# Performance work log

Measured on AMD Instinct MI355X. Metric: run time of the kernel, lower is better.

The kernel has to match this reference:

```python
import jax, jax.numpy as jnp
import numpy as np

NUM_SHARED = 2
NUM_EXPERTS = 8
NUM_LOCAL = NUM_EXPERTS - NUM_SHARED
TOP_K = 2
BALANCE_COEFF = 0.1
INPUT_DIM = 256
HIDDEN_DIM = 512
PRED_LEN = 256
NUM_SCALES = 3


def _gelu(v):
    return jax.nn.gelu(v, approximate=False)  # torch nn.GELU default = exact erf


def setup_inputs() -> dict:
    key = jax.random.key(0)
    ks = iter(jax.random.split(key, 32))
    s = 0.02

    def w(shape):
        return jax.random.normal(next(ks), shape, dtype=jnp.float32) * s

    inp = {}
    inp["xs"] = jax.random.normal(next(ks), (NUM_SCALES, 32, 512, INPUT_DIM), dtype=jnp.float32)
    # router: Linear(E, 2E) -> GELU -> Linear(2E, num_experts) -> softmax
    inp["router_w1"] = w((INPUT_DIM, 2 * INPUT_DIM)); inp["router_b1"] = jnp.zeros((2 * INPUT_DIM,), jnp.float32)
    inp["router_w2"] = w((2 * INPUT_DIM, NUM_EXPERTS)); inp["router_b2"] = jnp.zeros((NUM_EXPERTS,), jnp.float32)
    # global experts (3-layer MLP), stacked over num_shared
    inp["gW1"] = w((NUM_SHARED, INPUT_DIM, HIDDEN_DIM)); inp["gb1"] = jnp.zeros((NUM_SHARED, HIDDEN_DIM), jnp.float32)
    inp["gW2"] = w((NUM_SHARED, HIDDEN_DIM, HIDDEN_DIM)); inp["gb2"] = jnp.zeros((NUM_SHARED, HIDDEN_DIM), jnp.float32)
    inp["gW3"] = w((NUM_SHARED, HIDDEN_DIM, PRED_LEN)); inp["gb3"] = jnp.zeros((NUM_SHARED, PRED_LEN), jnp.float32)
    # local experts (2-layer MLP), stacked over num_local
    inp["lW1"] = w((NUM_LOCAL, INPUT_DIM, HIDDEN_DIM)); inp["lb1"] = jnp.zeros((NUM_LOCAL, HIDDEN_DIM), jnp.float32)
    inp["lW2"] = w((NUM_LOCAL, HIDDEN_DIM, PRED_LEN)); inp["lb2"] = jnp.zeros((NUM_LOCAL, PRED_LEN), jnp.float32)
    # TemporalAwareWeighting
    inp["te_w"] = w((PRED_LEN, PRED_LEN)); inp["te_b"] = jnp.zeros((PRED_LEN,), jnp.float32)
    inp["weight_memory"] = jnp.zeros((1, NUM_SCALES), jnp.float32)
    inp["wc_w"] = w((PRED_LEN * NUM_SCALES + NUM_SCALES, NUM_SCALES)); inp["wc_b"] = jnp.zeros((NUM_SCALES,), jnp.float32)
    # output layer
    inp["out_w1"] = w((PRED_LEN, PRED_LEN)); inp["out_b1"] = jnp.zeros((PRED_LEN,), jnp.float32)
    inp["out_w2"] = w((PRED_LEN, PRED_LEN)); inp["out_b2"] = jnp.zeros((PRED_LEN,), jnp.float32)
    return inp


def reference(xs, router_w1, router_b1, router_w2, router_b2,
              gW1, gb1, gW2, gb2, gW3, gb3,
              lW1, lb1, lW2, lb2,
              te_w, te_b, weight_memory, wc_w, wc_b,
              out_w1, out_b1, out_w2, out_b2):
    S, B, C, E = xs.shape
    x = xs.reshape(S, B * C, E)

    def scale_fwd(xf):  # xf: [T, E]
        h = _gelu(xf @ router_w1 + router_b1)
        w = jax.nn.softmax(h @ router_w2 + router_b2, axis=-1)  # [T, Ne]
        gw = w[:, :NUM_SHARED]
        lw, lidx = jax.lax.top_k(w[:, NUM_SHARED:], TOP_K)      # sorted desc, like torch.topk
        # global experts: all run, weighted sum
        gh = _gelu(jnp.einsum('te,seh->sth', xf, gW1) + gb1[:, None, :])
        gh = _gelu(jnp.einsum('sth,shg->stg', gh, gW2) + gb2[:, None, :])
        gout = jnp.einsum('stg,sgo->sto', gh, gW3) + gb3[:, None, :]   # [Ns, T, O]
        global_pred = jnp.einsum('sto,ts->to', gout, gw)
        # local experts: all run (as in source), then top-k gather
        lh = _gelu(jnp.einsum('te,neh->nth', xf, lW1) + lb1[:, None, :])
        lout = jnp.einsum('nth,nho->nto', lh, lW2) + lb2[:, None, :]   # [Nl, T, O]
        sel = jnp.take_along_axis(jnp.swapaxes(lout, 0, 1), lidx[:, :, None], axis=1)  # [T, k, O]
        local_pred = jnp.sum(sel * lw[:, :, None], axis=1)
        return global_pred + local_pred, w

    preds, all_w = jax.vmap(scale_fwd)(x)  # [S, T, O], [S, T, Ne]

    ws = all_w.reshape(-1, all_w.shape[-1])
    entropy = -jnp.mean(jnp.sum(ws * jnp.log(ws + 1e-8), axis=-1))
    balance_loss = BALANCE_COEFF * entropy

    preds_bc = preds.reshape(S, B, C, -1)
    # TemporalAwareWeighting (dropout = identity in eval)
    reprs = _gelu(jnp.mean(preds_bc, axis=2) @ te_w + te_b)            # [S, B, O]
    concat = jnp.transpose(reprs, (1, 0, 2)).reshape(B, -1)            # [B, S*O]
    mem = jnp.broadcast_to(weight_memory, (B, S))
    raw = jax.nn.softplus(jnp.tanh(jnp.concatenate([concat, mem], axis=-1) @ wc_w + wc_b))
    sw = jax.nn.softmax(raw, axis=-1)                                  # [B, S]

    weighted = jnp.einsum('sbco,bs->bco', preds_bc, sw)
    out = _gelu(weighted @ out_w1 + out_b1) @ out_w2 + out_b2
    return out, balance_loss
```

## Files before the change

kernel.cpp:

```cpp
#include <hip/hip_runtime.h>
#include <hip/hip_bf16.h>
#include <math.h>

#define S_   3
#define B_   32
#define C_   512
#define E_   256
#define H_   512
#define P_   256
#define T_   49152
#define TBC_ 16384

typedef __attribute__((ext_vector_type(8))) short v_s16x8;
typedef __attribute__((ext_vector_type(4))) float v_f32x4;

__device__ __forceinline__ float gelu_f(float x) {
  return 0.5f * x * (1.0f + erff(x * 0.70710678118654752440f));
}

__device__ __forceinline__ void gload_lds16(const void* g, void* l) {
  __builtin_amdgcn_global_load_lds((const __attribute__((address_space(1))) void*)g,
                                   (__attribute__((address_space(3))) void*)l, 16, 0, 0);
}

template<int MODE, bool STORE, bool SPLITA>
__global__ __launch_bounds__(256)
void gemm_bf16_k(const __hip_bfloat16* __restrict__ A,
                 const __hip_bfloat16* __restrict__ Bt,
                 const float* __restrict__ bias,
                 void* __restrict__ Cout,
                 const float* __restrict__ wtok,
                 int M, int N, int K, int eidx,
                 const __hip_bfloat16* __restrict__ Alo)
{
  __shared__ __align__(16) unsigned short As[4096];
  __shared__ __align__(16) unsigned short Bs[4096];
  const int tid  = threadIdx.x;
  const int wid  = tid >> 6;
  const int lane = tid & 63;
  const int wm = wid >> 1, wn = wid & 1;
  const int l15 = lane & 15, l4 = lane >> 4;

  v_f32x4 acc[4][4] = {};

  const size_t Kb   = (size_t)K * 2;
  const size_t ArsB = SPLITA ? 512 : Kb;
  const char* AgHi = (const char*)A + (size_t)blockIdx.x * 128 * ArsB;
  const char* AgLo = SPLITA ? ((const char*)Alo + (size_t)blockIdx.x * 128 * ArsB) : nullptr;
  const char* Bg   = (const char*)Bt + (size_t)blockIdx.y * 128 * Kb;

  const int ob0 = (0 * 4 + wid) * 1024 + lane * 16;
  const int ob1 = (1 * 4 + wid) * 1024 + lane * 16;
  const int r0 = ob0 >> 6, kb0 = ob0 & 63;
  const int r1 = ob1 >> 6, kb1 = ob1 & 63;
  char* lA0 = (char*)As + (0 * 4 + wid) * 1024;
  char* lA1 = (char*)As + (1 * 4 + wid) * 1024;
  char* lB0 = (char*)Bs + (0 * 4 + wid) * 1024;
  char* lB1 = (char*)Bs + (1 * 4 + wid) * 1024;
  const size_t aoff0 = (size_t)r0 * ArsB + kb0;
  const size_t aoff1 = (size_t)r1 * ArsB + kb1;
  const char* gB0 = Bg + (size_t)r0 * Kb + kb0;
  const char* gB1 = Bg + (size_t)r1 * Kb + kb1;

  for (int kt = 0; kt < K; kt += 32) {
    const char* Asrc = AgHi;
    size_t akt = (size_t)kt * 2;
    if (SPLITA) {
      akt = (size_t)(kt & 255) * 2;
      if ((kt >> 8) == 1) Asrc = AgLo;
    }
    size_t bkt = (size_t)kt * 2;
    gload_lds16(Asrc + aoff0 + akt, lA0);
    gload_lds16(Asrc + aoff1 + akt, lA1);
    gload_lds16(gB0 + bkt, lB0);
    gload_lds16(gB1 + bkt, lB1);
    __syncthreads();
    v_s16x8 af[4], bfv[4];
#pragma unroll
    for (int m = 0; m < 4; ++m)
      af[m] = *(const v_s16x8*)(As + (wm * 64 + m * 16 + l15) * 32 + l4 * 8);
#pragma unroll
    for (int n = 0; n < 4; ++n)
      bfv[n] = *(const v_s16x8*)(Bs + (wn * 64 + n * 16 + l15) * 32 + l4 * 8);
#pragma unroll
    for (int m = 0; m < 4; ++m)
#pragma unroll
      for (int n = 0; n < 4; ++n)
        acc[m][n] = __builtin_amdgcn_mfma_f32_16x16x32_bf16(af[m], bfv[n], acc[m][n], 0, 0, 0);
    __syncthreads();
  }

  const int crow0 = blockIdx.x * 128 + wm * 64;
  const int ccol0 = blockIdx.y * 128 + wn * 64;
#pragma unroll
  for (int m = 0; m < 4; ++m) {
    float wv[4];
    if (MODE == 1) {
#pragma unroll
      for (int j = 0; j < 4; ++j)
        wv[j] = wtok[(size_t)(crow0 + m * 16 + l4 * 4 + j) * 8 + eidx];
    }
#pragma unroll
    for (int n = 0; n < 4; ++n) {
      const int col = ccol0 + n * 16 + l15;
      const float bv = bias[col];
#pragma unroll
      for (int j = 0; j < 4; ++j) {
        const int row = crow0 + m * 16 + l4 * 4 + j;
        float v = acc[m][n][j] + bv;
        if (MODE == 0) {
          ((__hip_bfloat16*)Cout)[(size_t)row * N + col] = __float2bfloat16(gelu_f(v));
        } else if (MODE == 1) {
          float* Pp = (float*)Cout + (size_t)row * N + col;
          float val = v * wv[j];
          if (STORE) *Pp = val; else *Pp += val;
        } else if (MODE == 2) {
          ((float*)Cout)[(size_t)row * N + col] = v;
        } else {
          ((float*)Cout)[(size_t)row * N + col] = gelu_f(v);
        }
      }
    }
  }
}

__global__ __launch_bounds__(256) void logits_kernel(
    const float* __restrict__ hr,
    const float* __restrict__ w2,
    const float* __restrict__ b2,
    float* __restrict__ wtok,
    float* __restrict__ entp)
{
  const int t = blockIdx.x * 256 + threadIdx.x;
  const float4* hrow = (const float4*)(hr + (size_t)t * 512);
  float lg[8];
#pragma unroll
  for (int e = 0; e < 8; ++e) lg[e] = b2[e];
#pragma unroll 4
  for (int k4 = 0; k4 < 128; ++k4) {
    float4 hv = hrow[k4];
    float hvv[4] = {hv.x, hv.y, hv.z, hv.w};
#pragma unroll
    for (int j = 0; j < 4; ++j) {
      const float* wr = w2 + (k4 * 4 + j) * 8;
#pragma unroll
      for (int e = 0; e < 8; ++e) lg[e] += hvv[j] * wr[e];
    }
  }
  float we[8];
  float mx = lg[0];
#pragma unroll
  for (int e = 1; e < 8; ++e) mx = fmaxf(mx, lg[e]);
  float ssum = 0.f;
#pragma unroll
  for (int e = 0; e < 8; ++e) { we[e] = expf(lg[e] - mx); ssum += we[e]; }
#pragma unroll
  for (int e = 0; e < 8; ++e) we[e] = we[e] / ssum;
  float ent = 0.f;
#pragma unroll
  for (int e = 0; e < 8; ++e) ent += we[e] * logf(we[e] + 1e-8f);
  int i1 = 0; float v1 = we[2];
#pragma unroll
  for (int n = 1; n < 6; ++n) if (we[2 + n] > v1) { v1 = we[2 + n]; i1 = n; }
  int i2 = -1; float v2 = -1e30f;
#pragma unroll
  for (int n = 0; n < 6; ++n) if (n != i1 && we[2 + n] > v2) { v2 = we[2 + n]; i2 = n; }
  float ow[8];
  ow[0] = we[0]; ow[1] = we[1];
#pragma unroll
  for (int n = 0; n < 6; ++n) ow[2 + n] = 0.f;
  ow[2 + i1] = v1; ow[2 + i2] = v2;
  float* wp = wtok + (size_t)t * 8;
#pragma unroll
  for (int e = 0; e < 8; ++e) wp[e] = ow[e];
  __shared__ float red[256];
  red[threadIdx.x] = ent;
  __syncthreads();
  for (int s = 128; s > 0; s >>= 1) {
    if (threadIdx.x < s) red[threadIdx.x] += red[threadIdx.x + s];
    __syncthreads();
  }
  if (threadIdx.x == 0) atomicAdd(entp, red[0]);
}

__global__ void zero_kernel(float* p) { p[0] = 0.f; }

__global__ void convert_x_kernel(const float* __restrict__ x,
                                 __hip_bfloat16* __restrict__ xb,
                                 __hip_bfloat16* __restrict__ xlo, int n4) {
  int stride = gridDim.x * blockDim.x;
  for (int i = blockIdx.x * blockDim.x + threadIdx.x; i < n4; i += stride) {
    float4 v = ((const float4*)x)[i];
    float vv[4] = {v.x, v.y, v.z, v.w};
    union { __hip_bfloat16 h[4]; ushort4 u; } hi, lo;
#pragma unroll
    for (int j = 0; j < 4; ++j) {
      hi.h[j] = __float2bfloat16(vv[j]);
      lo.h[j] = __float2bfloat16(vv[j] - __bfloat162float(hi.h[j]));
    }
    ((ushort4*)xb)[i] = hi.u;
    ((ushort4*)xlo)[i] = lo.u;
  }
}

__global__ void build_router_w_kernel(const float* __restrict__ rw1,
                                      __hip_bfloat16* __restrict__ dst) {
  int i = blockIdx.x * 256 + threadIdx.x;
  int n = i / 768, k = i - n * 768;
  float src = rw1[(size_t)(k & 255) * 512 + n];
  __hip_bfloat16 hv = __float2bfloat16(src);
  dst[i] = (k < 512) ? hv : __float2bfloat16(src - __bfloat162float(hv));
}

struct ConvDesc { const float* src; __hip_bfloat16* dst; int K; int N; };
struct ConvArgs { ConvDesc d[20]; };

__global__ void convert_wt_kernel(ConvArgs a) {
  ConvDesc c = a.d[blockIdx.y];
  int total = c.K * c.N;
  int stride = gridDim.x * blockDim.x;
  for (int e = blockIdx.x * blockDim.x + threadIdx.x; e < total; e += stride) {
    int n = e / c.K;
    int k = e - n * c.K;
    c.dst[e] = __float2bfloat16(c.src[(size_t)k * c.N + n]);
  }
}

__global__ void mean_kernel(const float* __restrict__ pred, float* __restrict__ meanz) {
  int r = blockIdx.x, o = threadIdx.x;
  const float* p = pred + (size_t)r * 512 * 256 + o;
  float s0 = 0.f, s1 = 0.f, s2 = 0.f, s3 = 0.f;
  for (int c = 0; c < 512; c += 4) {
    s0 += p[(size_t)(c + 0) * 256]; s1 += p[(size_t)(c + 1) * 256];
    s2 += p[(size_t)(c + 2) * 256]; s3 += p[(size_t)(c + 3) * 256];
  }
  meanz[r * 256 + o] = (s0 + s1 + s2 + s3) * (1.0f / 512.0f);
}

__global__ void te_kernel(const float* __restrict__ meanz, const float* __restrict__ tw,
                          const float* __restrict__ tb, float* __restrict__ reprs) {
  __shared__ float row[256];
  int r = blockIdx.x, j = threadIdx.x;
  row[j] = meanz[r * 256 + j];
  __syncthreads();
  float a = 0.f;
  for (int k = 0; k < 256; ++k) a += row[k] * tw[k * 256 + j];
  reprs[r * 256 + j] = gelu_f(a + tb[j]);
}

__global__ void wc_kernel(const float* __restrict__ reprs, const float* __restrict__ wmem,
                          const float* __restrict__ wcw, const float* __restrict__ wcb,
                          float* __restrict__ sw) {
  __shared__ float red[128][3];
  int b = blockIdx.x, tid = threadIdx.x;
  float a0 = 0.f, a1 = 0.f, a2 = 0.f;
  for (int i = tid; i < 771; i += 128) {
    float cv = (i < 768) ? reprs[(i >> 8) * 8192 + b * 256 + (i & 255)] : wmem[i - 768];
    a0 += cv * wcw[i * 3 + 0]; a1 += cv * wcw[i * 3 + 1]; a2 += cv * wcw[i * 3 + 2];
  }
  red[tid][0] = a0; red[tid][1] = a1; red[tid][2] = a2;
  __syncthreads();
  for (int s = 64; s > 0; s >>= 1) {
    if (tid < s) {
      red[tid][0] += red[tid + s][0];
      red[tid][1] += red[tid + s][1];
      red[tid][2] += red[tid + s][2];
    }
    __syncthreads();
  }
  if (tid == 0) {
    float r[3]; float mx = -1e30f;
    for (int j = 0; j < 3; ++j) {
      float v = tanhf(red[0][j] + wcb[j]);
      r[j] = log1pf(expf(v));
      mx = fmaxf(mx, r[j]);
    }
    float s = 0.f;
    for (int j = 0; j < 3; ++j) { r[j] = expf(r[j] - mx); s += r[j]; }
    for (int j = 0; j < 3; ++j) sw[b * 3 + j] = r[j] / s;
  }
}

__global__ void weighted_kernel(const float* __restrict__ pred, const float* __restrict__ sw,
                                __hip_bfloat16* __restrict__ wb) {
  int t = blockIdx.x, o = threadIdx.x;
  int b = t >> 9;
  float s0 = sw[b * 3 + 0], s1 = sw[b * 3 + 1], s2 = sw[b * 3 + 2];
  size_t i = (size_t)t * 256 + o;
  float v = pred[i] * s0 + pred[i + (size_t)TBC_ * 256] * s1 + pred[i + (size_t)2 * TBC_ * 256] * s2;
  wb[i] = __float2bfloat16(v);
}

__global__ void finalize_kernel(const float* __restrict__ entp, float* __restrict__ out) {
  out[4194304] = -0.1f * entp[0] / 49152.0f;
}

extern "C" void kernel_launch(void* const* d_in, const int* in_sizes, int n_in,
                              void* d_out, int out_size, void* d_ws, size_t ws_size,
                              hipStream_t stream) {
  const float* x    = (const float*)d_in[0];
  const float* rw1  = (const float*)d_in[1];
  const float* rb1  = (const float*)d_in[2];
  const float* rw2  = (const float*)d_in[3];
  const float* rb2  = (const float*)d_in[4];
  const float* gW1  = (const float*)d_in[5];
  const float* gb1  = (const float*)d_in[6];
  const float* gW2  = (const float*)d_in[7];
  const float* gb2  = (const float*)d_in[8];
  const float* gW3  = (const float*)d_in[9];
  const float* gb3  = (const float*)d_in[10];
  const float* lW1  = (const float*)d_in[11];
  const float* lb1  = (const float*)d_in[12];
  const float* lW2  = (const float*)d_in[13];
  const float* lb2  = (const float*)d_in[14];
  const float* tew  = (const float*)d_in[15];
  const float* teb  = (const float*)d_in[16];
  const float* wmem = (const float*)d_in[17];
  const float* wcw  = (const float*)d_in[18];
  const float* wcb  = (const float*)d_in[19];
  const float* ow1  = (const float*)d_in[20];
  const float* ob1  = (const float*)d_in[21];
  const float* ow2  = (const float*)d_in[22];
  const float* ob2  = (const float*)d_in[23];
  float* out = (float*)d_out;

  char* ws = (char*)d_ws;
  size_t off = 0;
  auto alloc = [&](size_t bytes) -> void* {
    void* p = ws + off;
    off = (off + bytes + 255) & ~(size_t)255;
    return p;
  };
  __hip_bfloat16* Xb   = (__hip_bfloat16*)alloc((size_t)T_ * E_ * 2);
  __hip_bfloat16* Xlo  = (__hip_bfloat16*)alloc((size_t)T_ * E_ * 2);
  __hip_bfloat16* rW1s = (__hip_bfloat16*)alloc(512ull * 768 * 2);
  __hip_bfloat16* gW1t = (__hip_bfloat16*)alloc(2ull * H_ * E_ * 2);
  __hip_bfloat16* gW2t = (__hip_bfloat16*)alloc(2ull * H_ * H_ * 2);
  __hip_bfloat16* gW3t = (__hip_bfloat16*)alloc(2ull * P_ * H_ * 2);
  __hip_bfloat16* lW1t = (__hip_bfloat16*)alloc(6ull * H_ * E_ * 2);
  __hip_bfloat16* lW2t = (__hip_bfloat16*)alloc(6ull * P_ * H_ * 2);
  __hip_bfloat16* ow1t = (__hip_bfloat16*)alloc((size_t)P_ * E_ * 2);
  __hip_bfloat16* ow2t = (__hip_bfloat16*)alloc((size_t)P_ * P_ * 2);
  float* wtok  = (float*)alloc((size_t)T_ * 8 * 4);
  float* entp  = (float*)alloc(256);
  float* meanz = (float*)alloc(96ull * 256 * 4);
  float* reprs = (float*)alloc(96ull * 256 * 4);
  float* swp   = (float*)alloc(512);
  __hip_bfloat16* bufA = (__hip_bfloat16*)alloc((size_t)T_ * H_ * 2);
  __hip_bfloat16* bufB = (__hip_bfloat16*)alloc((size_t)T_ * H_ * 2);
  float* pred = (float*)alloc((size_t)T_ * P_ * 4);
  float* Hr = (float*)bufB;
  __hip_bfloat16* wghtB = bufA;
  __hip_bfloat16* out1B = bufB;

  ConvArgs ca;
  int d = 0;
  for (int s = 0; s < 2; ++s) ca.d[d++] = { gW1 + (size_t)s * E_ * H_, gW1t + (size_t)s * H_ * E_, E_, H_ };
  for (int s = 0; s < 2; ++s) ca.d[d++] = { gW2 + (size_t)s * H_ * H_, gW2t + (size_t)s * H_ * H_, H_, H_ };
  for (int s = 0; s < 2; ++s) ca.d[d++] = { gW3 + (size_t)s * H_ * P_, gW3t + (size_t)s * P_ * H_, H_, P_ };
  for (int n = 0; n < 6; ++n) ca.d[d++] = { lW1 + (size_t)n * E_ * H_, lW1t + (size_t)n * H_ * E_, E_, H_ };
  for (int n = 0; n < 6; ++n) ca.d[d++] = { lW2 + (size_t)n * H_ * P_, lW2t + (size_t)n * P_ * H_, H_, P_ };
  ca.d[d++] = { ow1, ow1t, E_, P_ };
  ca.d[d++] = { ow2, ow2t, P_, P_ };

  zero_kernel<<<1, 1, 0, stream>>>(entp);
  convert_x_kernel<<<1024, 256, 0, stream>>>(x, Xb, Xlo, T_ * E_ / 4);
  convert_wt_kernel<<<dim3(64, 20), 256, 0, stream>>>(ca);
  build_router_w_kernel<<<1536, 256, 0, stream>>>(rw1, rW1s);

  gemm_bf16_k<3, true, true><<<dim3(T_ / 128, 512 / 128), 256, 0, stream>>>(
      Xb, rW1s, rb1, Hr, nullptr, T_, 512, 768, 0, Xlo);
  logits_kernel<<<T_ / 256, 256, 0, stream>>>(Hr, rw2, rb2, wtok, entp);

  for (int s = 0; s < 2; ++s) {
    gemm_bf16_k<0, true, false><<<dim3(T_ / 128, H_ / 128), 256, 0, stream>>>(
        Xb, gW1t + (size_t)s * H_ * E_, gb1 + s * H_, bufA, nullptr, T_, H_, E_, 0, nullptr);
    gemm_bf16_k<0, true, false><<<dim3(T_ / 128, H_ / 128), 256, 0, stream>>>(
        bufA, gW2t + (size_t)s * H_ * H_, gb2 + s * H_, bufB, nullptr, T_, H_, H_, 0, nullptr);
    if (s == 0)
      gemm_bf16_k<1, true, false><<<dim3(T_ / 128, P_ / 128), 256, 0, stream>>>(
          bufB, gW3t + (size_t)s * P_ * H_, gb3 + s * P_, pred, wtok, T_, P_, H_, s, nullptr);
    else
      gemm_bf16_k<1, false, false><<<dim3(T_ / 128, P_ / 128), 256, 0, stream>>>(
          bufB, gW3t + (size_t)s * P_ * H_, gb3 + s * P_, pred, wtok, T_, P_, H_, s, nullptr);
  }
  for (int n = 0; n < 6; ++n) {
    gemm_bf16_k<0, true, false><<<dim3(T_ / 128, H_ / 128), 256, 0, stream>>>(
        Xb, lW1t + (size_t)n * H_ * E_, lb1 + n * H_, bufA, nullptr, T_, H_, E_, 0, nullptr);
    gemm_bf16_k<1, false, false><<<dim3(T_ / 128, P_ / 128), 256, 0, stream>>>(
        bufA, lW2t + (size_t)n * P_ * H_, lb2 + n * P_, pred, wtok, T_, P_, H_, 2 + n, nullptr);
  }

  mean_kernel<<<96, 256, 0, stream>>>(pred, meanz);
  te_kernel<<<96, 256, 0, stream>>>(meanz, tew, teb, reprs);
  wc_kernel<<<32, 128, 0, stream>>>(reprs, wmem, wcw, wcb, swp);
  weighted_kernel<<<TBC_, 256, 0, stream>>>(pred, swp, wghtB);

  gemm_bf16_k<0, true, false><<<dim3(TBC_ / 128, P_ / 128), 256, 0, stream>>>(
      wghtB, ow1t, ob1, out1B, nullptr, TBC_, P_, E_, 0, nullptr);
  gemm_bf16_k<2, true, false><<<dim3(TBC_ / 128, P_ / 128), 256, 0, stream>>>(
      out1B, ow2t, ob2, out, nullptr, TBC_, P_, P_, 0, nullptr);

  finalize_kernel<<<1, 1, 0, stream>>>(entp, out);
  (void)in_sizes; (void)n_in; (void)out_size; (void)ws_size;
}
```

Measured before the change: 1.022 ms.

## Batch expert GEMMs into wide concatenated GEMMs with fused gating epilogues

Concatenates the first-layer weights of all experts into wide 2048-column GEMMs. The router weight is pre-applied in the hidden activations, which lets the second-layer projections across experts collapse into two long-K GEMMs (K=2048) that accumulate directly into pred, with the weighted biases folded in through a shared-memory bias table. This cuts about 20 expert kernel launches to about 6, improves MXU/MFMA tile utilisation and removes repeated read-modify-write passes over the fp32 pred buffer. It needs a much larger workspace, so a fallback path keeps the old per-expert schedule when ws_size is below 440 MB. Pre-scaling by the gate weight before bf16 rounding slightly changes numerics.

After: 1.017 ms. Within noise of the previous version (-0.5%).

```diff
diff --git a/kernel.cpp b/kernel.cpp
--- a/kernel.cpp
+++ b/kernel.cpp
@@ -30,24 +30,32 @@
                  const float* __restrict__ bias,
                  void* __restrict__ Cout,
                  const float* __restrict__ wtok,
-                 int M, int N, int K, int eidx,
-                 const __hip_bfloat16* __restrict__ Alo)
+                 int M, int N, int K, int eidxBase,
+                 const __hip_bfloat16* __restrict__ Alo,
+                 int lda, int ldb, int ldc,
+                 __hip_bfloat16* __restrict__ Gout,
+                 const float* __restrict__ Ball)
 {
   __shared__ __align__(16) unsigned short As[4096];
   __shared__ __align__(16) unsigned short Bs[4096];
+  __shared__ float BallS[(MODE == 6 && STORE) ? 2048 : 1];
   const int tid  = threadIdx.x;
   const int wid  = tid >> 6;
   const int lane = tid & 63;
   const int wm = wid >> 1, wn = wid & 1;
   const int l15 = lane & 15, l4 = lane >> 4;
 
+  if constexpr (MODE == 6 && STORE) {
+    for (int i = tid; i < 2048; i += 256) BallS[i] = Ball[i];
+  }
+
   v_f32x4 acc[4][4] = {};
 
-  const size_t Kb   = (size_t)K * 2;
-  const size_t ArsB = SPLITA ? 512 : Kb;
+  const size_t ArsB = (size_t)lda * 2;
+  const size_t BrsB = (size_t)ldb * 2;
   const char* AgHi = (const char*)A + (size_t)blockIdx.x * 128 * ArsB;
   const char* AgLo = SPLITA ? ((const char*)Alo + (size_t)blockIdx.x * 128 * ArsB) : nullptr;
-  const char* Bg   = (const char*)Bt + (size_t)blockIdx.y * 128 * Kb;
+  const char* Bg   = (const char*)Bt + (size_t)blockIdx.y * 128 * BrsB;
 
   const int ob0 = (0 * 4 + wid) * 1024 + lane * 16;
   const int ob1 = (1 * 4 + wid) * 1024 + lane * 16;
@@ -59,8 +67,8 @@
   char* lB1 = (char*)Bs + (1 * 4 + wid) * 1024;
   const size_t aoff0 = (size_t)r0 * ArsB + kb0;
   const size_t aoff1 = (size_t)r1 * ArsB + kb1;
-  const char* gB0 = Bg + (size_t)r0 * Kb + kb0;
-  const char* gB1 = Bg + (size_t)r1 * Kb + kb1;
+  const char* gB0 = Bg + (size_t)r0 * BrsB + kb0;
+  const char* gB1 = Bg + (size_t)r1 * BrsB + kb1;
 
   for (int kt = 0; kt < K; kt += 32) {
     const char* Asrc = AgHi;
@@ -92,13 +100,55 @@
 
   const int crow0 = blockIdx.x * 128 + wm * 64;
   const int ccol0 = blockIdx.y * 128 + wn * 64;
+
+  if constexpr (MODE == 6) {
+    float* P = (float*)Cout;
+#pragma unroll
+    for (int m = 0; m < 4; ++m) {
+      float4 w0[4], w1[4];
+      if (STORE) {
+#pragma unroll
+        for (int j = 0; j < 4; ++j) {
+          const float4* wp = (const float4*)&wtok[(size_t)(crow0 + m * 16 + l4 * 4 + j) * 8];
+          w0[j] = wp[0]; w1[j] = wp[1];
+        }
+      }
+#pragma unroll
+      for (int n = 0; n < 4; ++n) {
+        const int col = ccol0 + n * 16 + l15;
+        float bs[8];
+        if (STORE) {
+#pragma unroll
+          for (int e = 0; e < 8; ++e) bs[e] = BallS[e * 256 + col];
+        }
+#pragma unroll
+        for (int j = 0; j < 4; ++j) {
+          const int row = crow0 + m * 16 + l4 * 4 + j;
+          float v = acc[m][n][j];
+          if (STORE) {
+            v += bs[0] * w0[j].x + bs[1] * w0[j].y + bs[2] * w0[j].z + bs[3] * w0[j].w
+               + bs[4] * w1[j].x + bs[5] * w1[j].y + bs[6] * w1[j].z + bs[7] * w1[j].w;
+            P[(size_t)row * ldc + col] = v;
+          } else {
+            P[(size_t)row * ldc + col] += v;
+          }
+        }
+      }
+    }
+    return;
+  }
+
 #pragma unroll
   for (int m = 0; m < 4; ++m) {
     float wv[4];
-    if (MODE == 1) {
+    if (MODE == 1 || MODE == 4 || MODE == 7) {
+      int e4 = 0;
+      if (MODE == 1) e4 = eidxBase;
+      if (MODE == 4) e4 = eidxBase + (ccol0 >> 9);
+      if (MODE == 7) e4 = (ccol0 >> 9);
 #pragma unroll
       for (int j = 0; j < 4; ++j)
-        wv[j] = wtok[(size_t)(crow0 + m * 16 + l4 * 4 + j) * 8 + eidx];
+        wv[j] = wtok[(size_t)(crow0 + m * 16 + l4 * 4 + j) * 8 + e4];
     }
 #pragma unroll
     for (int n = 0; n < 4; ++n) {
@@ -108,16 +158,24 @@
       for (int j = 0; j < 4; ++j) {
         const int row = crow0 + m * 16 + l4 * 4 + j;
         float v = acc[m][n][j] + bv;
-        if (MODE == 0) {
-          ((__hip_bfloat16*)Cout)[(size_t)row * N + col] = __float2bfloat16(gelu_f(v));
-        } else if (MODE == 1) {
-          float* Pp = (float*)Cout + (size_t)row * N + col;
+        if constexpr (MODE == 0) {
+          ((__hip_bfloat16*)Cout)[(size_t)row * ldc + col] = __float2bfloat16(gelu_f(v));
+        } else if constexpr (MODE == 1) {
+          float* Pp = (float*)Cout + (size_t)row * ldc + col;
           float val = v * wv[j];
           if (STORE) *Pp = val; else *Pp += val;
-        } else if (MODE == 2) {
-          ((float*)Cout)[(size_t)row * N + col] = v;
-        } else {
-          ((float*)Cout)[(size_t)row * N + col] = gelu_f(v);
+        } else if constexpr (MODE == 2) {
+          ((float*)Cout)[(size_t)row * ldc + col] = v;
+        } else if constexpr (MODE == 3) {
+          ((float*)Cout)[(size_t)row * ldc + col] = gelu_f(v);
+        } else if constexpr (MODE == 4) {
+          ((__hip_bfloat16*)Cout)[(size_t)row * ldc + col] = __float2bfloat16(wv[j] * gelu_f(v));
+        } else if constexpr (MODE == 7) {
+          if (ccol0 < 1024) {
+            Gout[(size_t)row * 1024 + col] = __float2bfloat16(gelu_f(v));
+          } else {
+            ((__hip_bfloat16*)Cout)[(size_t)row * ldc + col] = __float2bfloat16(wv[j] * gelu_f(v));
+          }
         }
       }
     }
@@ -212,7 +270,23 @@
   dst[i] = (k < 512) ? hv : __float2bfloat16(src - __bfloat162float(hv));
 }
 
-struct ConvDesc { const float* src; __hip_bfloat16* dst; int K; int N; };
+__global__ void build_biases_kernel(const float* __restrict__ gb1, const float* __restrict__ lb1,
+                                    const float* __restrict__ gb3, const float* __restrict__ lb2,
+                                    float* __restrict__ biasA, float* __restrict__ biasB,
+                                    float* __restrict__ Ball) {
+  int i = blockIdx.x * 256 + threadIdx.x;
+  if (i < 2048) {
+    biasA[i] = (i < 1024) ? gb1[i] : lb1[i - 1024];
+  } else if (i < 4096) {
+    int j = i - 2048;
+    biasB[j] = lb1[1024 + j];
+  } else {
+    int j = i - 4096;
+    Ball[j] = (j < 512) ? gb3[j] : lb2[j - 512];
+  }
+}
+
+struct ConvDesc { const float* src; __hip_bfloat16* dst; int K; int N; int ldb; int koff; };
 struct ConvArgs { ConvDesc d[20]; };
 
 __global__ void convert_wt_kernel(ConvArgs a) {
@@ -222,7 +296,7 @@
   for (int e = blockIdx.x * blockDim.x + threadIdx.x; e < total; e += stride) {
     int n = e / c.K;
     int k = e - n * c.K;
-    c.dst[e] = __float2bfloat16(c.src[(size_t)k * c.N + n]);
+    c.dst[(size_t)n * c.ldb + c.koff + k] = __float2bfloat16(c.src[(size_t)k * c.N + n]);
   }
 }
 
@@ -331,76 +405,138 @@
     off = (off + bytes + 255) & ~(size_t)255;
     return p;
   };
+
+  const bool batched = (ws_size >= (440ull << 20));
+
   __hip_bfloat16* Xb   = (__hip_bfloat16*)alloc((size_t)T_ * E_ * 2);
   __hip_bfloat16* Xlo  = (__hip_bfloat16*)alloc((size_t)T_ * E_ * 2);
   __hip_bfloat16* rW1s = (__hip_bfloat16*)alloc(512ull * 768 * 2);
-  __hip_bfloat16* gW1t = (__hip_bfloat16*)alloc(2ull * H_ * E_ * 2);
-  __hip_bfloat16* gW2t = (__hip_bfloat16*)alloc(2ull * H_ * H_ * 2);
-  __hip_bfloat16* gW3t = (__hip_bfloat16*)alloc(2ull * P_ * H_ * 2);
-  __hip_bfloat16* lW1t = (__hip_bfloat16*)alloc(6ull * H_ * E_ * 2);
-  __hip_bfloat16* lW2t = (__hip_bfloat16*)alloc(6ull * P_ * H_ * 2);
-  __hip_bfloat16* ow1t = (__hip_bfloat16*)alloc((size_t)P_ * E_ * 2);
-  __hip_bfloat16* ow2t = (__hip_bfloat16*)alloc((size_t)P_ * P_ * 2);
   float* wtok  = (float*)alloc((size_t)T_ * 8 * 4);
   float* entp  = (float*)alloc(256);
   float* meanz = (float*)alloc(96ull * 256 * 4);
   float* reprs = (float*)alloc(96ull * 256 * 4);
   float* swp   = (float*)alloc(512);
-  __hip_bfloat16* bufA = (__hip_bfloat16*)alloc((size_t)T_ * H_ * 2);
-  __hip_bfloat16* bufB = (__hip_bfloat16*)alloc((size_t)T_ * H_ * 2);
-  float* pred = (float*)alloc((size_t)T_ * P_ * 4);
-  float* Hr = (float*)bufB;
-  __hip_bfloat16* wghtB = bufA;
-  __hip_bfloat16* out1B = bufB;
-
-  ConvArgs ca;
-  int d = 0;
-  for (int s = 0; s < 2; ++s) ca.d[d++] = { gW1 + (size_t)s * E_ * H_, gW1t + (size_t)s * H_ * E_, E_, H_ };
-  for (int s = 0; s < 2; ++s) ca.d[d++] = { gW2 + (size_t)s * H_ * H_, gW2t + (size_t)s * H_ * H_, H_, H_ };
-  for (int s = 0; s < 2; ++s) ca.d[d++] = { gW3 + (size_t)s * H_ * P_, gW3t + (size_t)s * P_ * H_, H_, P_ };
-  for (int n = 0; n < 6; ++n) ca.d[d++] = { lW1 + (size_t)n * E_ * H_, lW1t + (size_t)n * H_ * E_, E_, H_ };
-  for (int n = 0; n < 6; ++n) ca.d[d++] = { lW2 + (size_t)n * H_ * P_, lW2t + (size_t)n * P_ * H_, H_, P_ };
-  ca.d[d++] = { ow1, ow1t, E_, P_ };
-  ca.d[d++] = { ow2, ow2t, P_, P_ };
+  __hip_bfloat16* ow1t = (__hip_bfloat16*)alloc((size_t)P_ * E_ * 2);
+  __hip_bfloat16* ow2t = (__hip_bfloat16*)alloc((size_t)P_ * P_ * 2);
 
   zero_kernel<<<1, 1, 0, stream>>>(entp);
   convert_x_kernel<<<1024, 256, 0, stream>>>(x, Xb, Xlo, T_ * E_ / 4);
-  convert_wt_kernel<<<dim3(64, 20), 256, 0, stream>>>(ca);
   build_router_w_kernel<<<1536, 256, 0, stream>>>(rw1, rW1s);
 
-  gemm_bf16_k<3, true, true><<<dim3(T_ / 128, 512 / 128), 256, 0, stream>>>(
-      Xb, rW1s, rb1, Hr, nullptr, T_, 512, 768, 0, Xlo);
-  logits_kernel<<<T_ / 256, 256, 0, stream>>>(Hr, rw2, rb2, wtok, entp);
-
-  for (int s = 0; s < 2; ++s) {
-    gemm_bf16_k<0, true, false><<<dim3(T_ / 128, H_ / 128), 256, 0, stream>>>(
-        Xb, gW1t + (size_t)s * H_ * E_, gb1 + s * H_, bufA, nullptr, T_, H_, E_, 0, nullptr);
-    gemm_bf16_k<0, true, false><<<dim3(T_ / 128, H_ / 128), 256, 0, stream>>>(
-        bufA, gW2t + (size_t)s * H_ * H_, gb2 + s * H_, bufB, nullptr, T_, H_, H_, 0, nullptr);
-    if (s == 0)
-      gemm_bf16_k<1, true, false><<<dim3(T_ / 128, P_ / 128), 256, 0, stream>>>(
-          bufB, gW3t + (size_t)s * P_ * H_, gb3 + s * P_, pred, wtok, T_, P_, H_, s, nullptr);
-    else
-      gemm_bf16_k<1, false, false><<<dim3(T_ / 128, P_ / 128), 256, 0, stream>>>(
-          bufB, gW3t + (size_t)s * P_ * H_, gb3 + s * P_, pred, wtok, T_, P_, H_, s, nullptr);
-  }
-  for (int n = 0; n < 6; ++n) {
-    gemm_bf16_k<0, true, false><<<dim3(T_ / 128, H_ / 128), 256, 0, stream>>>(
-        Xb, lW1t + (size_t)n * H_ * E_, lb1 + n * H_, bufA, nullptr, T_, H_, E_, 0, nullptr);
-    gemm_bf16_k<1, false, false><<<dim3(T_ / 128, P_ / 128), 256, 0, stream>>>(
-        bufA, lW2t + (size_t)n * P_ * H_, lb2 + n * P_, pred, wtok, T_, P_, H_, 2 + n, nullptr);
-  }
-
-  mean_kernel<<<96, 256, 0, stream>>>(pred, meanz);
-  te_kernel<<<96, 256, 0, stream>>>(meanz, tew, teb, reprs);
-  wc_kernel<<<32, 128, 0, stream>>>(reprs, wmem, wcw, wcb, swp);
-  weighted_kernel<<<TBC_, 256, 0, stream>>>(pred, swp, wghtB);
-
-  gemm_bf16_k<0, true, false><<<dim3(TBC_ / 128, P_ / 128), 256, 0, stream>>>(
-      wghtB, ow1t, ob1, out1B, nullptr, TBC_, P_, E_, 0, nullptr);
-  gemm_bf16_k<2, true, false><<<dim3(TBC_ / 128, P_ / 128), 256, 0, stream>>>(
-      out1B, ow2t, ob2, out, nullptr, TBC_, P_, P_, 0, nullptr);
+  if (batched) {
+    __hip_bfloat16* Bt1a = (__hip_bfloat16*)alloc(2048ull * 256 * 2);
+    __hip_bfloat16* Bt1b = (__hip_bfloat16*)alloc(2048ull * 256 * 2);
+    __hip_bfloat16* gW2t = (__hip_bfloat16*)alloc(2ull * H_ * H_ * 2);
+    __hip_bfloat16* Bf1  = (__hip_bfloat16*)alloc(256ull * 2048 * 2);
+    __hip_bfloat16* Bf2  = (__hip_bfloat16*)alloc(256ull * 2048 * 2);
+    float* biasA = (float*)alloc(2048 * 4);
+    float* biasB = (float*)alloc(2048 * 4);
+    float* Ball  = (float*)alloc(2048 * 4);
+    __hip_bfloat16* Ap = (__hip_bfloat16*)alloc((size_t)T_ * 2048 * 2);
+    __hip_bfloat16* G  = (__hip_bfloat16*)alloc((size_t)T_ * 1024 * 2);
+    float* pred = (float*)alloc((size_t)T_ * P_ * 4);
+    float* Hr = (float*)Ap;
+    __hip_bfloat16* wghtB = Xlo;
+    __hip_bfloat16* out1B = Xlo + (size_t)TBC_ * 256;
+
+    ConvArgs ca;
+    int d = 0;
+    for (int s = 0; s < 2; ++s) ca.d[d++] = { gW1 + (size_t)s * E_ * H_, Bt1a + (size_t)s * 512 * 256, E_, H_, 256, 0 };
+    for (int n = 0; n < 2; ++n) ca.d[d++] = { lW1 + (size_t)n * E_ * H_, Bt1a + (size_t)(2 + n) * 512 * 256, E_, H_, 256, 0 };
+    for (int n = 2; n < 6; ++n) ca.d[d++] = { lW1 + (size_t)n * E_ * H_, Bt1b + (size_t)(n - 2) * 512 * 256, E_, H_, 256, 0 };
+    for (int s = 0; s < 2; ++s) ca.d[d++] = { gW2 + (size_t)s * H_ * H_, gW2t + (size_t)s * H_ * H_, H_, H_, 512, 0 };
+    for (int s = 0; s < 2; ++s) ca.d[d++] = { gW3 + (size_t)s * H_ * P_, Bf1, H_, P_, 2048, s * 512 };
+    for (int n = 0; n < 2; ++n) ca.d[d++] = { lW2 + (size_t)n * H_ * P_, Bf1, H_, P_, 2048, (2 + n) * 512 };
+    for (int n = 2; n < 6; ++n) ca.d[d++] = { lW2 + (size_t)n * H_ * P_, Bf2, H_, P_, 2048, (n - 2) * 512 };
+    ca.d[d++] = { ow1, ow1t, E_, P_, 256, 0 };
+    ca.d[d++] = { ow2, ow2t, P_, P_, 256, 0 };
+    convert_wt_kernel<<<dim3(64, d), 256, 0, stream>>>(ca);
+    build_biases_kernel<<<24, 256, 0, stream>>>(gb1, lb1, gb3, lb2, biasA, biasB, Ball);
+
+    gemm_bf16_k<3, true, true><<<dim3(T_ / 128, 4), 256, 0, stream>>>(
+        Xb, rW1s, rb1, Hr, nullptr, T_, 512, 768, 0, Xlo, 256, 768, 512, nullptr, nullptr);
+    logits_kernel<<<T_ / 256, 256, 0, stream>>>(Hr, rw2, rb2, wtok, entp);
+
+    gemm_bf16_k<7, true, false><<<dim3(T_ / 128, 16), 256, 0, stream>>>(
+        Xb, Bt1a, biasA, Ap, wtok, T_, 2048, 256, 0, nullptr, 256, 256, 2048, G, nullptr);
+    for (int s = 0; s < 2; ++s)
+      gemm_bf16_k<4, true, false><<<dim3(T_ / 128, 4), 256, 0, stream>>>(
+          G + (size_t)s * 512, gW2t + (size_t)s * H_ * H_, gb2 + s * H_,
+          Ap + (size_t)s * 512, wtok, T_, 512, 512, s, nullptr, 1024, 512, 2048, nullptr, nullptr);
+    gemm_bf16_k<6, true, false><<<dim3(T_ / 128, 2), 256, 0, stream>>>(
+        Ap, Bf1, nullptr, pred, wtok, T_, 256, 2048, 0, nullptr, 2048, 2048, 256, nullptr, Ball);
+    gemm_bf16_k<4, true, false><<<dim3(T_ / 128, 16), 256, 0, stream>>>(
+        Xb, Bt1b, biasB, Ap, wtok, T_, 2048, 256, 4, nullptr, 256, 256, 2048, nullptr, nullptr);
+    gemm_bf16_k<6, false, false><<<dim3(T_ / 128, 2), 256, 0, stream>>>(
+        Ap, Bf2, nullptr, pred, wtok, T_, 256, 2048, 0, nullptr, 2048, 2048, 256, nullptr, nullptr);
+
+    mean_kernel<<<96, 256, 0, stream>>>(pred, meanz);
+    te_kernel<<<96, 256, 0, stream>>>(meanz, tew, teb, reprs);
+    wc_kernel<<<32, 128, 0, stream>>>(reprs, wmem, wcw, wcb, swp);
+    weighted_kernel<<<TBC_, 256, 0, stream>>>(pred, swp, wghtB);
+
+    gemm_bf16_k<0, true, false><<<dim3(TBC_ / 128, 2), 256, 0, stream>>>(
+        wghtB, ow1t, ob1, out1B, nullptr, TBC_, 256, 256, 0, nullptr, 256, 256, 256, nullptr, nullptr);
+    gemm_bf16_k<2, true, false><<<dim3(TBC_ / 128, 2), 256, 0, stream>>>(
+        out1B, ow2t, ob2, out, nullptr, TBC_, 256, 256, 0, nullptr, 256, 256, 256, nullptr, nullptr);
+  } else {
+    __hip_bfloat16* gW1t = (__hip_bfloat16*)alloc(2ull * H_ * E_ * 2);
+    __hip_bfloat16* gW2t = (__hip_bfloat16*)alloc(2ull * H_ * H_ * 2);
+    __hip_bfloat16* gW3t = (__hip_bfloat16*)alloc(2ull * P_ * H_ * 2);
+    __hip_bfloat16* lW1t = (__hip_bfloat16*)alloc(6ull * H_ * E_ * 2);
+    __hip_bfloat16* lW2t = (__hip_bfloat16*)alloc(6ull * P_ * H_ * 2);
+    __hip_bfloat16* bufA = (__hip_bfloat16*)alloc((size_t)T_ * H_ * 2);
+    __hip_bfloat16* bufB = (__hip_bfloat16*)alloc((size_t)T_ * H_ * 2);
+    float* pred = (float*)alloc((size_t)T_ * P_ * 4);
+    float* Hr = (float*)bufB;
+    __hip_bfloat16* wghtB = bufA;
+    __hip_bfloat16* out1B = bufB;
+
+    ConvArgs ca;
+    int d = 0;
+    for (int s = 0; s < 2; ++s) ca.d[d++] = { gW1 + (size_t)s * E_ * H_, gW1t + (size_t)s * H_ * E_, E_, H_, 256, 0 };
+    for (int s = 0; s < 2; ++s) ca.d[d++] = { gW2 + (size_t)s * H_ * H_, gW2t + (size_t)s * H_ * H_, H_, H_, 512, 0 };
+    for (int s = 0; s < 2; ++s) ca.d[d++] = { gW3 + (size_t)s * H_ * P_, gW3t + (size_t)s * P_ * H_, H_, P_, 512, 0 };
+    for (int n = 0; n < 6; ++n) ca.d[d++] = { lW1 + (size_t)n * E_ * H_, lW1t + (size_t)n * H_ * E_, E_, H_, 256, 0 };
+    for (int n = 0; n < 6; ++n) ca.d[d++] = { lW2 + (size_t)n * H_ * P_, lW2t + (size_t)n * P_ * H_, H_, P_, 512, 0 };
+    ca.d[d++] = { ow1, ow1t, E_, P_, 256, 0 };
+    ca.d[d++] = { ow2, ow2t, P_, P_, 256, 0 };
+    convert_wt_kernel<<<dim3(64, d), 256, 0, stream>>>(ca);
+
+    gemm_bf16_k<3, true, true><<<dim3(T_ / 128, 4), 256, 0, stream>>>(
+        Xb, rW1s, rb1, Hr, nullptr, T_, 512, 768, 0, Xlo, 256, 768, 512, nullptr, nullptr);
+    logits_kernel<<<T_ / 256, 256, 0, stream>>>(Hr, rw2, rb2, wtok, entp);
+
+    for (int s = 0; s < 2; ++s) {
+      gemm_bf16_k<0, true, false><<<dim3(T_ / 128, 4), 256, 0, stream>>>(
+          Xb, gW1t + (size_t)s * H_ * E_, gb1 + s * H_, bufA, nullptr, T_, 512, 256, 0, nullptr, 256, 256, 512, nullptr, nullptr);
+      gemm_bf16_k<0, true, false><<<dim3(T_ / 128, 4), 256, 0, stream>>>(
+          bufA, gW2t + (size_t)s * H_ * H_, gb2 + s * H_, bufB, nullptr, T_, 512, 512, 0, nullptr, 512, 512, 512, nullptr, nullptr);
+      if (s == 0)
+        gemm_bf16_k<1, true, false><<<dim3(T_ / 128, 2), 256, 0, stream>>>(
+            bufB, gW3t + (size_t)s * P_ * H_, gb3 + s * P_, pred, wtok, T_, 256, 512, s, nullptr, 512, 512, 256, nullptr, nullptr);
+      else
+        gemm_bf16_k<1, false, false><<<dim3(T_ / 128, 2), 256, 0, stream>>>(
+            bufB, gW3t + (size_t)s * P_ * H_, gb3 + s * P_, pred, wtok, T_, 256, 512, s, nullptr, 512, 512, 256, nullptr, nullptr);
+    }
+    for (int n = 0; n < 6; ++n) {
+      gemm_bf16_k<0, true, false><<<dim3(T_ / 128, 4), 256, 0, stream>>>(
+          Xb, lW1t + (size_t)n * H_ * E_, lb1 + n * H_, bufA, nullptr, T_, 512, 256, 0, nullptr, 256, 256, 512, nullptr, nullptr);
+      gemm_bf16_k<1, false, false><<<dim3(T_ / 128, 2), 256, 0, stream>>>(
+          bufA, lW2t + (size_t)n * P_ * H_, lb2 + n * P_, pred, wtok, T_, 256, 512, 2 + n, nullptr, 512, 512, 256, nullptr, nullptr);
+    }
+
+    mean_kernel<<<96, 256, 0, stream>>>(pred, meanz);
+    te_kernel<<<96, 256, 0, stream>>>(meanz, tew, teb, reprs);
+    wc_kernel<<<32, 128, 0, stream>>>(reprs, wmem, wcw, wcb, swp);
+    weighted_kernel<<<TBC_, 256, 0, stream>>>(pred, swp, wghtB);
+
+    gemm_bf16_k<0, true, false><<<dim3(TBC_ / 128, 2), 256, 0, stream>>>(
+        wghtB, ow1t, ob1, out1B, nullptr, TBC_, 256, 256, 0, nullptr, 256, 256, 256, nullptr, nullptr);
+    gemm_bf16_k<2, true, false><<<dim3(TBC_ / 128, 2), 256, 0, stream>>>(
+        out1B, ow2t, ob2, out, nullptr, TBC_, 256, 256, 0, nullptr, 256, 256, 256, nullptr, nullptr);
+  }
 
   finalize_kernel<<<1, 1, 0, stream>>>(entp, out);
-  (void)in_sizes; (void)n_in; (void)out_size; (void)ws_size;
-}
+  (void)in_sizes; (void)n_in; (void)out_size;
+}
```
